# Kernel tuning notes

Measured on AMD Instinct MI355X. Metric: run time of the kernel, lower is better.

The kernel has to match this reference:

```python
import jax, jax.numpy as jnp
import numpy as np

KS = 3          # ksize
PAD = 1         # (ksize-1)//2 * dilation, dilation=1

def setup_inputs() -> dict:
    key = jax.random.key(0)
    k1, k2, k3, k4 = jax.random.split(key, 4)
    B, NI, C, H, W = 4, 64, 64, 256, 256
    features = jax.random.normal(k1, (B, NI, H, W), jnp.float32)
    inpt = jax.random.normal(k2, (B, C, H, W), jnp.float32)
    # get_filter: Conv2d(ni, ksize**2, 3, padding=1 reflect, stride=1)
    w = jax.random.normal(k3, (KS * KS, NI, 3, 3), jnp.float32) * 0.05
    b = jax.random.normal(k4, (KS * KS,), jnp.float32) * 0.01
    return {"features": features, "inpt": inpt, "w": w, "b": b}

def reference(features, inpt, w, b):
    # 1) predict per-pixel filters: 3x3 conv with reflect padding
    fpad = jnp.pad(features, ((0, 0), (0, 0), (1, 1), (1, 1)), mode="reflect")
    ff = jax.lax.conv_general_dilated(
        fpad, w, window_strides=(1, 1), padding="VALID",
        dimension_numbers=("NCHW", "OIHW", "NCHW"),
    ) + b[None, :, None, None]                       # [B, 9, H, W]
    ff = jax.nn.softmax(ff, axis=1)                  # softmax over the 9 taps

    # 2) apply per-pixel filter to inpt (shared across channels)
    B, C, H, W = inpt.shape
    ipad = jnp.pad(inpt, ((0, 0), (0, 0), (PAD, PAD), (PAD, PAD)), mode="reflect")
    # unfold: taps in row-major (ki, kj) order, matching torch nn.Unfold
    patches = jnp.stack(
        [ipad[:, :, i:i + H, j:j + W] for i in range(KS) for j in range(KS)],
        axis=2,
    )                                                # [B, C, 9, H, W]
    # out[b,c,h,w] = sum_k patches[b,c,k,h,w] * ff[b,k,h,w]
    return jnp.einsum("bckhw,bkhw->bchw", patches, ff)
```

## Files before the change

### kernel.cpp

```cpp
#include <hip/hip_runtime.h>
#include <math.h>

#define BB 4
#define NIC 64
#define CC 64
#define HH 256
#define WW 256
#define HW (HH * WW)

typedef short sh8 __attribute__((ext_vector_type(8)));
typedef float f32x4 __attribute__((ext_vector_type(4)));

__device__ __forceinline__ int refl(int i, int n) {
    i = (i < 0) ? -i : i;
    return (i >= n) ? (2 * n - 2 - i) : i;
}
__device__ __forceinline__ unsigned short f2bf(float v) {
    unsigned int x = __builtin_bit_cast(unsigned int, v);
    return (unsigned short)((x + 0x7FFFu + ((x >> 16) & 1u)) >> 16);
}

__global__ void pff_prep(const float* __restrict__ wgt, uint4* __restrict__ wtab) {
    int e = blockIdx.x * 256 + threadIdx.x;
    if (e >= 1152) return;
    const int c = e >> 6, l = e & 63;
    const int p = c / 9, s = c - p * 9;
    const int tap = l & 15, kg = l >> 4;
    unsigned short h[8];
    #pragma unroll
    for (int j = 0; j < 8; ++j) {
        const int ni = 32 * p + 8 * kg + j;
        const float v = (tap <= 8) ? wgt[tap * 576 + ni * 9 + s] : 0.f;
        h[j] = f2bf(v);
    }
    uint4 o;
    o.x = h[0] | ((unsigned)h[1] << 16);
    o.y = h[2] | ((unsigned)h[3] << 16);
    o.z = h[4] | ((unsigned)h[5] << 16);
    o.w = h[6] | ((unsigned)h[7] << 16);
    wtab[e] = o;
}

__global__ __launch_bounds__(512) void pff_hyb(
    const float* __restrict__ features,
    const float* __restrict__ inpt,
    const float* __restrict__ bias,
    const uint4* __restrict__ wtab,
    float* __restrict__ out)
{
    __shared__ float lds[11220];
    __shared__ float ffl[9 * 512];

    const int tid = threadIdx.x;
    const int wv  = __builtin_amdgcn_readfirstlane(tid >> 6);
    const int l   = tid & 63;
    const int pxl = l & 15, kg = l >> 4;
    const int W0 = blockIdx.x * 64, H0 = blockIdx.y * 8, b = blockIdx.z;

    unsigned short* FT = (unsigned short*)lds;

    f32x4 acc[4];
    #pragma unroll
    for (int g = 0; g < 4; ++g) acc[g] = (f32x4){0.f, 0.f, 0.f, 0.f};

    const int bfbase = (wv * 66 + pxl) * 34 + kg * 8;

    #pragma unroll
    for (int p = 0; p < 2; ++p) {
        uint4 wf[9];
        #pragma unroll
        for (int s = 0; s < 9; ++s) wf[s] = wtab[(p * 9 + s) * 64 + l];

        for (int i = 0; i < 21; ++i) {
            const int flat = tid + 512 * i;
            if (flat < 10560) {
                const int nip = flat / 660;
                const int rc  = flat - nip * 660;
                const int r   = rc / 66, c2 = rc - r * 66;
                const int gr = refl(H0 - 1 + r, HH), gc = refl(W0 - 1 + c2, WW);
                const float* fp = features
                    + ((size_t)b * NIC + 32 * p + 2 * nip) * HW + gr * WW + gc;
                const unsigned pk = f2bf(fp[0]) | ((unsigned)f2bf(fp[HW]) << 16);
                *(unsigned*)&FT[(r * 66 + c2) * 34 + 2 * nip] = pk;
            }
        }
        __syncthreads();

        #pragma unroll
        for (int g = 0; g < 4; ++g) {
            #pragma unroll
            for (int s = 0; s < 9; ++s) {
                const int di = s / 3, dj = s - di * 3;
                const unsigned* q =
                    (const unsigned*)&FT[bfbase + (di * 66 + 16 * g + dj) * 34];
                uint4 bw;
                bw.x = q[0]; bw.y = q[1]; bw.z = q[2]; bw.w = q[3];
                acc[g] = __builtin_amdgcn_mfma_f32_16x16x32_bf16(
                    __builtin_bit_cast(sh8, wf[s]),
                    __builtin_bit_cast(sh8, bw), acc[g], 0, 0, 0);
            }
        }
        __syncthreads();
    }

    float bv4[4];
    #pragma unroll
    for (int j = 0; j < 4; ++j) {
        const int tap = 4 * kg + j;
        bv4[j] = bias[tap <= 8 ? tap : 8];
    }
    #pragma unroll
    for (int g = 0; g < 4; ++g) {
        float lg[4]; bool val[4];
        #pragma unroll
        for (int j = 0; j < 4; ++j) {
            const int tap = 4 * kg + j;
            val[j] = (tap <= 8);
            lg[j] = acc[g][j] + bv4[j];
        }
        float ml = -3e38f;
        #pragma unroll
        for (int j = 0; j < 4; ++j) ml = fmaxf(ml, val[j] ? lg[j] : -3e38f);
        float m = fmaxf(ml, __shfl_xor(ml, 16));
        m = fmaxf(m, __shfl_xor(m, 32));
        float e[4], sl = 0.f;
        #pragma unroll
        for (int j = 0; j < 4; ++j) { e[j] = val[j] ? __expf(lg[j] - m) : 0.f; sl += e[j]; }
        float s = sl + __shfl_xor(sl, 16);
        s += __shfl_xor(s, 32);
        const float inv = 1.f / s;
        #pragma unroll
        for (int j = 0; j < 4; ++j)
            if (val[j]) ffl[(4 * kg + j) * 512 + wv * 64 + 16 * g + pxl] = e[j] * inv;
    }

    const int q2 = wv >> 1, tw = wv & 1;
    const int R0 = H0 + 4 * tw;
    int goff[7], loff[7]; bool dm[7];
    #pragma unroll
    for (int t = 0; t < 7; ++t) {
        const int e = l + 64 * t;
        dm[t] = (e < 396);
        const int row = e / 66, col = e - row * 66;
        loff[t] = row * 68 + col;
        goff[t] = refl(R0 - 1 + row, HH) * WW + refl(W0 - 1 + col, WW);
    }
    const float* ip = inpt + ((size_t)b * CC + q2 * 16) * HW;
    float r[7];
    #pragma unroll
    for (int t = 0; t < 7; ++t) r[t] = dm[t] ? ip[goff[t]] : 0.f;

    __syncthreads();

    float ffv[9][4];
    #pragma unroll
    for (int k = 0; k < 9; ++k)
        #pragma unroll
        for (int rr = 0; rr < 4; ++rr)
            ffv[k][rr] = ffl[k * 512 + (4 * tw + rr) * 64 + l];

    float* sb = lds + wv * 816;
    float* ob = out + ((size_t)b * CC + q2 * 16) * HW;

    for (int ch = 0; ch < 16; ++ch) {
        float* s2 = sb + (ch & 1) * 408;
        #pragma unroll
        for (int t = 0; t < 7; ++t) if (dm[t]) s2[loff[t]] = r[t];
        if (ch < 15) {
            const float* in2 = ip + (size_t)(ch + 1) * HW;
            #pragma unroll
            for (int t = 0; t < 7; ++t) r[t] = dm[t] ? in2[goff[t]] : 0.f;
        }

        float f[3][6];
        #pragma unroll
        for (int dc = 0; dc < 3; ++dc)
            #pragma unroll
            for (int row = 0; row < 6; ++row)
                f[dc][row] = s2[row * 68 + l + dc];

        float* op = ob + (size_t)ch * HW + R0 * WW + W0 + l;
        #pragma unroll
        for (int rr = 0; rr < 4; ++rr) {
            float o = ffv[0][rr] * f[0][rr];
            o = fmaf(ffv[1][rr], f[1][rr],     o);
            o = fmaf(ffv[2][rr], f[2][rr],     o);
            o = fmaf(ffv[3][rr], f[0][rr + 1], o);
            o = fmaf(ffv[4][rr], f[1][rr + 1], o);
            o = fmaf(ffv[5][rr], f[2][rr + 1], o);
            o = fmaf(ffv[6][rr], f[0][rr + 2], o);
            o = fmaf(ffv[7][rr], f[1][rr + 2], o);
            o = fmaf(ffv[8][rr], f[2][rr + 2], o);
            op[rr * WW] = o;
        }
    }
}

extern "C" void kernel_launch(void* const* d_in, const int* in_sizes, int n_in,
                              void* d_out, int out_size, void* d_ws, size_t ws_size,
                              hipStream_t stream) {
    const float* features = (const float*)d_in[0];
    const float* inpt     = (const float*)d_in[1];
    const float* wgt      = (const float*)d_in[2];
    const float* bias     = (const float*)d_in[3];
    float* out            = (float*)d_out;
    uint4* wtab           = (uint4*)d_ws;

    pff_prep<<<dim3(5), dim3(256), 0, stream>>>(wgt, wtab);

    dim3 grid(WW / 64, HH / 8, BB);
    dim3 block(512);
    pff_hyb<<<grid, block, 0, stream>>>(features, inpt, bias, wtab, out);
}
```

Before: 76.48 us.

## Shrink tile to 32-wide and apply filters from registers with float4 global loads

The spatial tile shrinks from 64x8 to 32x8 pixels, doubling the grid and cutting LDS use, which should raise occupancy. The filter-application stage no longer stages input rows through LDS. Each lane now loads float4 rows plus halo scalars straight from global memory, prefetches the next channel, and writes float4 outputs, with each wave handling 8 channels. Staging offsets are precomputed and the final barrier is dropped. The cost is more redundant halo reads of features and inpt across the smaller tiles.

```diff
diff --git a/kernel.cpp b/kernel.cpp
--- a/kernel.cpp
+++ b/kernel.cpp
@@ -41,29 +41,37 @@
     wtab[e] = o;
 }
 
-__global__ __launch_bounds__(512) void pff_hyb(
+__global__ __launch_bounds__(512) void pff_fuse3(
     const float* __restrict__ features,
     const float* __restrict__ inpt,
     const float* __restrict__ bias,
     const uint4* __restrict__ wtab,
     float* __restrict__ out)
 {
-    __shared__ float lds[11220];
-    __shared__ float ffl[9 * 512];
+    __shared__ unsigned short FT[10 * 34 * 34];
+    __shared__ float ffl[9 * 256];
 
     const int tid = threadIdx.x;
     const int wv  = __builtin_amdgcn_readfirstlane(tid >> 6);
     const int l   = tid & 63;
     const int pxl = l & 15, kg = l >> 4;
-    const int W0 = blockIdx.x * 64, H0 = blockIdx.y * 8, b = blockIdx.z;
-
-    unsigned short* FT = (unsigned short*)lds;
-
-    f32x4 acc[4];
-    #pragma unroll
-    for (int g = 0; g < 4; ++g) acc[g] = (f32x4){0.f, 0.f, 0.f, 0.f};
-
-    const int bfbase = (wv * 66 + pxl) * 34 + kg * 8;
+    const int W0 = blockIdx.x * 32, H0 = blockIdx.y * 8, b = blockIdx.z;
+
+    int stg_g[11], stg_l[11];
+    #pragma unroll
+    for (int i = 0; i < 11; ++i) {
+        const int flat = tid + 512 * i;
+        const int nip = flat / 340;
+        const int rc  = flat - nip * 340;
+        const int r   = rc / 34, c2 = rc - r * 34;
+        stg_l[i] = (flat < 5440) ? ((r * 34 + c2) * 34 + 2 * nip) : -1;
+        stg_g[i] = refl(H0 - 1 + r, HH) * WW + refl(W0 - 1 + c2, WW)
+                 + 2 * nip * HW;
+    }
+
+    f32x4 acc[2];
+    acc[0] = (f32x4){0.f, 0.f, 0.f, 0.f};
+    acc[1] = (f32x4){0.f, 0.f, 0.f, 0.f};
 
     #pragma unroll
     for (int p = 0; p < 2; ++p) {
@@ -71,28 +79,24 @@
         #pragma unroll
         for (int s = 0; s < 9; ++s) wf[s] = wtab[(p * 9 + s) * 64 + l];
 
-        for (int i = 0; i < 21; ++i) {
-            const int flat = tid + 512 * i;
-            if (flat < 10560) {
-                const int nip = flat / 660;
-                const int rc  = flat - nip * 660;
-                const int r   = rc / 66, c2 = rc - r * 66;
-                const int gr = refl(H0 - 1 + r, HH), gc = refl(W0 - 1 + c2, WW);
-                const float* fp = features
-                    + ((size_t)b * NIC + 32 * p + 2 * nip) * HW + gr * WW + gc;
+        const float* fp0 = features + ((size_t)b * NIC + 32 * p) * HW;
+        #pragma unroll
+        for (int i = 0; i < 11; ++i) {
+            if (stg_l[i] >= 0) {
+                const float* fp = fp0 + stg_g[i];
                 const unsigned pk = f2bf(fp[0]) | ((unsigned)f2bf(fp[HW]) << 16);
-                *(unsigned*)&FT[(r * 66 + c2) * 34 + 2 * nip] = pk;
+                *(unsigned*)&FT[stg_l[i]] = pk;
             }
         }
         __syncthreads();
 
         #pragma unroll
-        for (int g = 0; g < 4; ++g) {
+        for (int g = 0; g < 2; ++g) {
             #pragma unroll
             for (int s = 0; s < 9; ++s) {
                 const int di = s / 3, dj = s - di * 3;
-                const unsigned* q =
-                    (const unsigned*)&FT[bfbase + (di * 66 + 16 * g + dj) * 34];
+                const unsigned* q = (const unsigned*)
+                    &FT[((wv + di) * 34 + pxl + 16 * g + dj) * 34 + kg * 8];
                 uint4 bw;
                 bw.x = q[0]; bw.y = q[1]; bw.z = q[2]; bw.w = q[3];
                 acc[g] = __builtin_amdgcn_mfma_f32_16x16x32_bf16(
@@ -100,7 +104,7 @@
                     __builtin_bit_cast(sh8, bw), acc[g], 0, 0, 0);
             }
         }
-        __syncthreads();
+        if (p == 0) __syncthreads();
     }
 
     float bv4[4];
@@ -110,7 +114,7 @@
         bv4[j] = bias[tap <= 8 ? tap : 8];
     }
     #pragma unroll
-    for (int g = 0; g < 4; ++g) {
+    for (int g = 0; g < 2; ++g) {
         float lg[4]; bool val[4];
         #pragma unroll
         for (int j = 0; j < 4; ++j) {
@@ -130,68 +134,92 @@
         s += __shfl_xor(s, 32);
         const float inv = 1.f / s;
         #pragma unroll
-        for (int j = 0; j < 4; ++j)
-            if (val[j]) ffl[(4 * kg + j) * 512 + wv * 64 + 16 * g + pxl] = e[j] * inv;
-    }
-
-    const int q2 = wv >> 1, tw = wv & 1;
-    const int R0 = H0 + 4 * tw;
-    int goff[7], loff[7]; bool dm[7];
-    #pragma unroll
-    for (int t = 0; t < 7; ++t) {
-        const int e = l + 64 * t;
-        dm[t] = (e < 396);
-        const int row = e / 66, col = e - row * 66;
-        loff[t] = row * 68 + col;
-        goff[t] = refl(R0 - 1 + row, HH) * WW + refl(W0 - 1 + col, WW);
-    }
-    const float* ip = inpt + ((size_t)b * CC + q2 * 16) * HW;
-    float r[7];
-    #pragma unroll
-    for (int t = 0; t < 7; ++t) r[t] = dm[t] ? ip[goff[t]] : 0.f;
-
+        for (int j = 0; j < 4; ++j) {
+            const int tap = 4 * kg + j;
+            if (val[j]) ffl[tap * 256 + wv * 32 + 16 * g + pxl] = e[j] * inv;
+        }
+    }
     __syncthreads();
 
-    float ffv[9][4];
-    #pragma unroll
-    for (int k = 0; k < 9; ++k)
-        #pragma unroll
-        for (int rr = 0; rr < 4; ++rr)
-            ffv[k][rr] = ffl[k * 512 + (4 * tw + rr) * 64 + l];
-
-    float* sb = lds + wv * 816;
-    float* ob = out + ((size_t)b * CC + q2 * 16) * HW;
-
-    for (int ch = 0; ch < 16; ++ch) {
-        float* s2 = sb + (ch & 1) * 408;
-        #pragma unroll
-        for (int t = 0; t < 7; ++t) if (dm[t]) s2[loff[t]] = r[t];
-        if (ch < 15) {
-            const float* in2 = ip + (size_t)(ch + 1) * HW;
-            #pragma unroll
-            for (int t = 0; t < 7; ++t) r[t] = dm[t] ? in2[goff[t]] : 0.f;
-        }
-
-        float f[3][6];
-        #pragma unroll
-        for (int dc = 0; dc < 3; ++dc)
-            #pragma unroll
-            for (int row = 0; row < 6; ++row)
-                f[dc][row] = s2[row * 68 + l + dc];
-
-        float* op = ob + (size_t)ch * HW + R0 * WW + W0 + l;
-        #pragma unroll
-        for (int rr = 0; rr < 4; ++rr) {
-            float o = ffv[0][rr] * f[0][rr];
-            o = fmaf(ffv[1][rr], f[1][rr],     o);
-            o = fmaf(ffv[2][rr], f[2][rr],     o);
-            o = fmaf(ffv[3][rr], f[0][rr + 1], o);
-            o = fmaf(ffv[4][rr], f[1][rr + 1], o);
-            o = fmaf(ffv[5][rr], f[2][rr + 1], o);
-            o = fmaf(ffv[6][rr], f[0][rr + 2], o);
-            o = fmaf(ffv[7][rr], f[1][rr + 2], o);
-            o = fmaf(ffv[8][rr], f[2][rr + 2], o);
-            op[rr * WW] = o;
+    const int lr = l >> 3;
+    const int k4 = (l & 7) << 2;
+
+    float4 fq[9];
+    #pragma unroll
+    for (int t = 0; t < 9; ++t)
+        fq[t] = *(const float4*)&ffl[t * 256 + lr * 32 + k4];
+
+    int gr[3];
+    #pragma unroll
+    for (int i = 0; i < 3; ++i) gr[i] = refl(H0 + lr - 1 + i, HH) * WW;
+    const int c0 = W0 + k4;
+    const int cL = refl(c0 - 1, WW);
+    const int cR = refl(c0 + 4, WW);
+
+    const float* ip = inpt + ((size_t)b * CC + wv * 8) * HW;
+    float* op = out + ((size_t)b * CC + wv * 8) * HW + (size_t)(H0 + lr) * WW + c0;
+
+    float4 v0 = *(const float4*)&ip[gr[0] + c0];
+    float4 v1 = *(const float4*)&ip[gr[1] + c0];
+    float4 v2 = *(const float4*)&ip[gr[2] + c0];
+    float e0 = ip[gr[0] + cL], e1 = ip[gr[1] + cL], e2 = ip[gr[2] + cL];
+    float d0 = ip[gr[0] + cR], d1 = ip[gr[1] + cR], d2 = ip[gr[2] + cR];
+
+    for (int ch = 0; ch < 8; ++ch) {
+        float4 n0, n1, n2; float m0, m1, m2, p0, p1, p2;
+        if (ch < 7) {
+            const float* i2 = ip + (size_t)(ch + 1) * HW;
+            n0 = *(const float4*)&i2[gr[0] + c0];
+            n1 = *(const float4*)&i2[gr[1] + c0];
+            n2 = *(const float4*)&i2[gr[2] + c0];
+            m0 = i2[gr[0] + cL]; m1 = i2[gr[1] + cL]; m2 = i2[gr[2] + cL];
+            p0 = i2[gr[0] + cR]; p1 = i2[gr[1] + cR]; p2 = i2[gr[2] + cR];
+        }
+
+        float4 o;
+        o.x =      fq[0].x * e0;
+        o.x = fmaf(fq[1].x, v0.x, o.x);
+        o.x = fmaf(fq[2].x, v0.y, o.x);
+        o.x = fmaf(fq[3].x, e1,   o.x);
+        o.x = fmaf(fq[4].x, v1.x, o.x);
+        o.x = fmaf(fq[5].x, v1.y, o.x);
+        o.x = fmaf(fq[6].x, e2,   o.x);
+        o.x = fmaf(fq[7].x, v2.x, o.x);
+        o.x = fmaf(fq[8].x, v2.y, o.x);
+        o.y =      fq[0].y * v0.x;
+        o.y = fmaf(fq[1].y, v0.y, o.y);
+        o.y = fmaf(fq[2].y, v0.z, o.y);
+        o.y = fmaf(fq[3].y, v1.x, o.y);
+        o.y = fmaf(fq[4].y, v1.y, o.y);
+        o.y = fmaf(fq[5].y, v1.z, o.y);
+        o.y = fmaf(fq[6].y, v2.x, o.y);
+        o.y = fmaf(fq[7].y, v2.y, o.y);
+        o.y = fmaf(fq[8].y, v2.z, o.y);
+        o.z =      fq[0].z * v0.y;
+        o.z = fmaf(fq[1].z, v0.z, o.z);
+        o.z = fmaf(fq[2].z, v0.w, o.z);
+        o.z = fmaf(fq[3].z, v1.y, o.z);
+        o.z = fmaf(fq[4].z, v1.z, o.z);
+        o.z = fmaf(fq[5].z, v1.w, o.z);
+        o.z = fmaf(fq[6].z, v2.y, o.z);
+        o.z = fmaf(fq[7].z, v2.z, o.z);
+        o.z = fmaf(fq[8].z, v2.w, o.z);
+        o.w =      fq[0].w * v0.z;
+        o.w = fmaf(fq[1].w, v0.w, o.w);
+        o.w = fmaf(fq[2].w, d0,   o.w);
+        o.w = fmaf(fq[3].w, v1.z, o.w);
+        o.w = fmaf(fq[4].w, v1.w, o.w);
+        o.w = fmaf(fq[5].w, d1,   o.w);
+        o.w = fmaf(fq[6].w, v2.z, o.w);
+        o.w = fmaf(fq[7].w, v2.w, o.w);
+        o.w = fmaf(fq[8].w, d2,   o.w);
+
+        *(float4*)&op[(size_t)ch * HW] = o;
+
+        if (ch < 7) {
+            v0 = n0; v1 = n1; v2 = n2;
+            e0 = m0; e1 = m1; e2 = m2;
+            d0 = p0; d1 = p1; d2 = p2;
         }
     }
 }
@@ -208,7 +236,7 @@
 
     pff_prep<<<dim3(5), dim3(256), 0, stream>>>(wgt, wtab);
 
-    dim3 grid(WW / 64, HH / 8, BB);
+    dim3 grid(WW / 32, HH / 8, BB);
     dim3 block(512);
-    pff_hyb<<<grid, block, 0, stream>>>(features, inpt, bias, wtab, out);
-}
+    pff_fuse3<<<grid, block, 0, stream>>>(features, inpt, bias, wtab, out);
+}
```

Measured after the change: 78.53 us. 1.03x slower.
